# Optimization experiments

Measured on AMD Instinct MI355X. Metric: run time of the kernel, lower is better.

Reference implementation:

```python
import jax, jax.numpy as jnp
import numpy as np

NUM_CLASSES = 21
RMI_RADIUS = 3
POOL = 3            # rmi_pool_size == rmi_pool_stride
HALF_D = RMI_RADIUS * RMI_RADIUS
WEIGHT_LAMBDA = 0.5
CLIP_MIN = 1e-6
POS_ALPHA = 5e-4


def _max_pool(x):
    # F.max_pool2d(kernel=3, stride=3, padding=1) on NCHW
    return jax.lax.reduce_window(
        x, -jnp.inf, jax.lax.max,
        window_dimensions=(1, 1, POOL, POOL),
        window_strides=(1, 1, POOL, POOL),
        padding=[(0, 0), (0, 0), (1, 1), (1, 1)])


def _map_get_pairs(labels, probs, radius):
    # -> two tensors [N, C, radius*radius, new_h, new_w]
    h, w = labels.shape[2], labels.shape[3]
    nh, nw = h - (radius - 1), w - (radius - 1)
    la = jnp.stack([labels[:, :, y:y + nh, x:x + nw]
                    for y in range(radius) for x in range(radius)], axis=2)
    pr = jnp.stack([probs[:, :, y:y + nh, x:x + nw]
                    for y in range(radius) for x in range(radius)], axis=2)
    return la, pr


def _rmi_lower_bound(labels_4D, probs_4D):
    labels_4D = _max_pool(labels_4D)
    probs_4D = _max_pool(probs_4D)
    la, pr = _map_get_pairs(labels_4D, probs_4D, RMI_RADIUS)
    N, C = la.shape[0], la.shape[1]
    la = jax.lax.stop_gradient(la.reshape(N, C, HALF_D, -1))  # [N,C,D,M]
    pr = pr.reshape(N, C, HALF_D, -1)
    la = la - jnp.mean(la, axis=3, keepdims=True)
    pr = pr - jnp.mean(pr, axis=3, keepdims=True)
    eye = jnp.eye(HALF_D, dtype=pr.dtype) * POS_ALPHA  # broadcast over N,C
    la_cov = jnp.einsum('ncdm,ncem->ncde', la, la)
    pr_cov = jnp.einsum('ncdm,ncem->ncde', pr, pr)
    pr_cov_inv = jnp.linalg.inv(pr_cov + eye)
    la_pr_cov = jnp.einsum('ncdm,ncem->ncde', la, pr)
    appro_var = la_cov - jnp.einsum('ncde,ncef,ncgf->ncdg',
                                    la_pr_cov, pr_cov_inv, la_pr_cov)
    chol = jnp.linalg.cholesky(appro_var + eye)
    diag = jnp.diagonal(chol, axis1=-2, axis2=-1)
    rmi_now = 0.5 * 2.0 * jnp.sum(jnp.log(diag + 1e-8), axis=-1)  # [N,C]
    rmi_per_class = jnp.mean(rmi_now.reshape(-1, NUM_CLASSES), axis=0) / float(HALF_D)
    return jnp.sum(rmi_per_class)  # _IS_SUM = 1


def setup_inputs() -> dict:
    key = jax.random.key(0)
    k1, k2 = jax.random.split(key)
    logits_4D = jax.random.normal(k1, (4, NUM_CLASSES, 512, 512), dtype=jnp.float32)
    labels_4D = jax.random.randint(k2, (4, 512, 512), 0, NUM_CLASSES).astype(jnp.int64)
    return {'logits_4D': logits_4D, 'labels_4D': labels_4D}


def reference(logits_4D, labels_4D):
    # forward_sigmoid
    mask = (labels_4D < NUM_CLASSES)                       # [N,H,W] bool
    maskf = mask.astype(logits_4D.dtype)
    onehot = jax.nn.one_hot(labels_4D * mask, NUM_CLASSES,
                            dtype=logits_4D.dtype) * maskf[..., None]  # [N,H,W,C]
    onehot = jax.lax.stop_gradient(onehot)
    logits_flat = jnp.transpose(logits_4D, (0, 2, 3, 1)).reshape(-1, NUM_CLASSES)
    y_flat = onehot.reshape(-1, NUM_CLASSES)
    w_flat = maskf.reshape(-1, 1)
    valid_pixels = jnp.sum(maskf)
    # stable BCE-with-logits, sum reduction, per-pixel weight
    bce = -(y_flat * jax.nn.log_sigmoid(logits_flat)
            + (1.0 - y_flat) * jax.nn.log_sigmoid(-logits_flat))
    bce_loss = jnp.sum(bce * w_flat) / (valid_pixels + 1.0)
    probs_4D = jax.nn.sigmoid(logits_4D) * maskf[:, None, :, :] + CLIP_MIN
    labels_nchw = jnp.transpose(onehot, (0, 3, 1, 2))
    rmi_loss = _rmi_lower_bound(labels_nchw, probs_4D)
    # lambda_way == 1
    return WEIGHT_LAMBDA * bce_loss + rmi_loss * (1.0 - WEIGHT_LAMBDA)
```

## Files before the change

kernel.cpp:

```cpp
#include <hip/hip_runtime.h>
#include <math.h>
#include <stdint.h>

#define NUM_CL 21
#define NB 4
#define H 512
#define W 512
#define PH 171
#define PW 171
#define PWPAD 176
#define NHH 169
#define NWW 169
#define M_TOT (NHH*NWW)
#define NCP (NB*NUM_CL)
#define ACC_PAD 192
#define POS_ALPHA 5e-4
#define NBLKA (NB*NUM_CL*PH)
#define NROWBLK (NB*PH)
#define SEGR 43

typedef unsigned long long u64;
typedef unsigned int u32;

__device__ __forceinline__ int upIdx(int lo, int hi) {
    return lo*9 - (lo*(lo-1))/2 + (hi - lo);
}
__device__ __forceinline__ int tri(int d, int e) { return d*(d+1)/2 + e; }

__device__ __forceinline__ float wred64(float v) {
    #pragma unroll
    for (int o = 32; o > 0; o >>= 1) v += __shfl_down(v, o, 64);
    return v;
}

__global__ __launch_bounds__(128) void kernelA(
    const float* __restrict__ logits, const int* __restrict__ labels,
    float* __restrict__ pooledP, unsigned char* __restrict__ pooledL8,
    float* __restrict__ bce_part, u32* __restrict__ cnt_part)
{
    int blk = blockIdx.x;
    int c  = blk % NUM_CL;
    int t2 = blk / NUM_CL;
    int ph = t2 % PH;
    int n  = t2 / PH;
    int tid = threadIdx.x;
    int col0 = tid << 2;

    __shared__ float         svP[W];
    __shared__ unsigned char svL[W];
    __shared__ float         rbce[2];
    __shared__ u32           rcnt[2];

    const float* lgp = logits + (size_t)(n*NUM_CL + c) * (H*W);
    const int*   lbp = labels + (size_t)n * (H*W);

    float vP[4] = {-INFINITY, -INFINITY, -INFINITY, -INFINITY};
    int   vL[4] = {0,0,0,0};
    float bce = 0.f;
    u32 cnt = 0;

    int rbase = 3*ph - 1;
    #pragma unroll
    for (int rr = 0; rr < 3; ++rr) {
        int r = rbase + rr;
        if (r < 0 || r >= H) continue;
        float4 x4 = *(const float4*)(lgp + (size_t)r*W + col0);
        int4   l4 = *(const int4*)  (lbp + (size_t)r*W + col0);
        float xs[4] = {x4.x, x4.y, x4.z, x4.w};
        int   ls[4] = {l4.x, l4.y, l4.z, l4.w};
        #pragma unroll
        for (int k = 0; k < 4; ++k) {
            int lab = ls[k];
            float x = xs[k];
            float m = (lab < NUM_CL) ? 1.f : 0.f;
            float y = (lab == c) ? 1.f : 0.f;
            float te = __expf(-fabsf(x));
            float u  = 1.f + te;
            float sp = __logf(u);
            float rc = __builtin_amdgcn_rcpf(u);
            bce += m * (fmaxf(x, 0.f) - x*y + sp);
            float sig = (x >= 0.f) ? rc : te*rc;
            vP[k] = fmaxf(vP[k], sig*m + 1e-6f);
            vL[k] |= (lab == c);
            cnt += (u32)(lab < NUM_CL);
        }
    }

    ((float4*)svP)[tid] = make_float4(vP[0], vP[1], vP[2], vP[3]);
    uchar4 u4;
    u4.x = (unsigned char)vL[0]; u4.y = (unsigned char)vL[1];
    u4.z = (unsigned char)vL[2]; u4.w = (unsigned char)vL[3];
    ((uchar4*)svL)[tid] = u4;

    #pragma unroll
    for (int o = 32; o > 0; o >>= 1) {
        bce += __shfl_down(bce, o, 64);
        cnt += __shfl_down(cnt, o, 64);
    }
    int lane = tid & 63, wv = tid >> 6;
    if (lane == 0) { rbce[wv] = bce; rcnt[wv] = cnt; }
    __syncthreads();

    size_t rowr = (size_t)(n*NUM_CL + c) * PH + ph;
    #pragma unroll
    for (int pass = 0; pass < 2; ++pass) {
        int pw = tid + pass*128;
        if (pw < PW) {
            int c0 = 3*pw - 1; if (c0 < 0) c0 = 0;
            int c1 = 3*pw + 2; if (c1 > W) c1 = W;
            float pm = -INFINITY;
            int lm = 0;
            for (int qq = c0; qq < c1; ++qq) {
                pm = fmaxf(pm, svP[qq]);
                lm |= svL[qq];
            }
            pooledP [rowr * PWPAD + pw] = pm;
            pooledL8[rowr * PWPAD + pw] = (unsigned char)lm;
        }
    }

    if (tid == 0) {
        bce_part[blk] = rbce[0] + rbce[1];
        if (c == 0) cnt_part[t2] = rcnt[0] + rcnt[1];
    }
}

template<int CNT>
__device__ __forceinline__ void blockReduceStore(
    float (&v)[CNT], float* __restrict__ stage, int off, bool active,
    int lane, int wave)
{
    __shared__ float red[4][CNT];
    #pragma unroll
    for (int k = 0; k < CNT; ++k) {
        float r = wred64(active ? v[k] : 0.f);
        if (lane == 0) red[wave][k] = r;
    }
    __syncthreads();
    for (int k = (int)threadIdx.x; k < CNT; k += 256) {
        stage[off + k] = red[0][k] + red[1][k] + red[2][k] + red[3][k];
    }
    __syncthreads();
}

__global__ __launch_bounds__(256, 1) void kernelB(
    const float* __restrict__ pooledP, const unsigned char* __restrict__ pooledL8,
    float* __restrict__ stage)
{
    int nc    = blockIdx.x;
    int chunk = blockIdx.y;
    int grp   = blockIdx.z;
    int lane  = threadIdx.x & 63;
    int seg   = threadIdx.x >> 6;
    int j     = chunk*64 + lane;
    bool active = (j < NWW);
    int jc = active ? j : (NWW - 1);
    int i0 = seg * SEGR;
    int i1 = (seg == 3) ? NWW : (i0 + SEGR);

    const float* P = pooledP + (size_t)nc * PH * PWPAD + jc;
    const unsigned char* L = pooledL8 + (size_t)nc * PH * PWPAD + jc;
    float* st = stage + (size_t)(nc*3 + chunk) * ACC_PAD;

    float pA[3], pB[3], lA[3], lB[3];
    #pragma unroll
    for (int t = 0; t < 3; ++t) {
        pA[t] = P[(size_t)i0 * PWPAD + t];
        lA[t] = (float)L[(size_t)i0 * PWPAD + t];
        pB[t] = P[(size_t)(i0+1) * PWPAD + t];
        lB[t] = (float)L[(size_t)(i0+1) * PWPAD + t];
    }

    if (grp == 0) {
        float sl[9], sp[9], cll[45], cpp[45];
        #pragma unroll
        for (int d = 0; d < 9; ++d) { sl[d] = 0.f; sp[d] = 0.f; }
        #pragma unroll
        for (int k = 0; k < 45; ++k) { cll[k] = 0.f; cpp[k] = 0.f; }

        for (int i = i0; i < i1; ++i) {
            const float* rp = P + (size_t)(i+2) * PWPAD;
            const unsigned char* rl = L + (size_t)(i+2) * PWPAD;
            float pC[3] = {rp[0], rp[1], rp[2]};
            float lC[3] = {(float)rl[0], (float)rl[1], (float)rl[2]};
            float pv[9] = {pA[0],pA[1],pA[2], pB[0],pB[1],pB[2], pC[0],pC[1],pC[2]};
            float lv[9] = {lA[0],lA[1],lA[2], lB[0],lB[1],lB[2], lC[0],lC[1],lC[2]};
            #pragma unroll
            for (int d = 0; d < 9; ++d) { sp[d] += pv[d]; sl[d] += lv[d]; }
            int k = 0;
            #pragma unroll
            for (int d = 0; d < 9; ++d)
                #pragma unroll
                for (int e = d; e < 9; ++e) {
                    cpp[k] += pv[d]*pv[e];
                    cll[k] += lv[d]*lv[e];
                    ++k;
                }
            #pragma unroll
            for (int t = 0; t < 3; ++t) {
                pA[t] = pB[t]; pB[t] = pC[t];
                lA[t] = lB[t]; lB[t] = lC[t];
            }
        }
        blockReduceStore<9> (sl,  st, 0,  active, lane, seg);
        blockReduceStore<9> (sp,  st, 9,  active, lane, seg);
        blockReduceStore<45>(cll, st, 18, active, lane, seg);
        blockReduceStore<45>(cpp, st, 63, active, lane, seg);
    } else {
        float clp[81];
        #pragma unroll
        for (int k = 0; k < 81; ++k) clp[k] = 0.f;

        for (int i = i0; i < i1; ++i) {
            const float* rp = P + (size_t)(i+2) * PWPAD;
            const unsigned char* rl = L + (size_t)(i+2) * PWPAD;
            float pC[3] = {rp[0], rp[1], rp[2]};
            float lC[3] = {(float)rl[0], (float)rl[1], (float)rl[2]};
            float pv[9] = {pA[0],pA[1],pA[2], pB[0],pB[1],pB[2], pC[0],pC[1],pC[2]};
            float lv[9] = {lA[0],lA[1],lA[2], lB[0],lB[1],lB[2], lC[0],lC[1],lC[2]};
            #pragma unroll
            for (int d = 0; d < 9; ++d)
                #pragma unroll
                for (int e = 0; e < 9; ++e)
                    clp[d*9+e] += lv[d]*pv[e];
            #pragma unroll
            for (int t = 0; t < 3; ++t) {
                pA[t] = pB[t]; pB[t] = pC[t];
                lA[t] = lB[t]; lB[t] = lC[t];
            }
        }
        blockReduceStore<81>(clp, st, 108, active, lane, seg);
    }
}

__device__ __forceinline__ double rdacc(const float* __restrict__ st, int t, int k) {
    const float* b = st + (size_t)t * 3 * ACC_PAD + k;
    return (double)b[0] + (double)b[ACC_PAD] + (double)b[2*ACC_PAD];
}

__global__ __launch_bounds__(256) void kernelC(
    const float* __restrict__ stage,
    const float* __restrict__ bce_part,
    const u32* __restrict__ cnt_part,
    float* __restrict__ out)
{
    int t = threadIdx.x;

    __shared__ double sb[256];
    __shared__ u32 sc[256];
    double bs = 0.0;
    for (int i = t; i < NBLKA; i += 256) bs += (double)bce_part[i];
    u32 cs = 0;
    for (int i = t; i < NROWBLK; i += 256) cs += cnt_part[i];
    sb[t] = bs; sc[t] = cs;
    __syncthreads();
    #pragma unroll
    for (int s = 128; s > 0; s >>= 1) {
        if (t < s) { sb[t] += sb[t + s]; sc[t] += sc[t + s]; }
        __syncthreads();
    }

    float contrib = 0.f;
    if (t < NCP) {
        const double Minv = 1.0 / (double)M_TOT;
        double Sl[9], Sp[9];
        #pragma unroll
        for (int d = 0; d < 9; ++d) { Sl[d] = rdacc(stage, t, d); Sp[d] = rdacc(stage, t, 9+d); }

        float A[45];
        float G[45];
        float B[81];
        #pragma unroll
        for (int d = 0; d < 9; ++d) {
            #pragma unroll
            for (int e = 0; e <= d; ++e) {
                int ku = upIdx(e, d);
                double vp = rdacc(stage, t, 63+ku) - Sp[d]*Sp[e]*Minv;
                double vl = rdacc(stage, t, 18+ku) - Sl[d]*Sl[e]*Minv;
                if (d == e) vp += POS_ALPHA;
                A[tri(d,e)] = (float)vp;
                G[tri(d,e)] = (float)vl;
            }
        }
        #pragma unroll
        for (int d = 0; d < 9; ++d) {
            #pragma unroll
            for (int e = 0; e < 9; ++e)
                B[d*9+e] = (float)(rdacc(stage, t, 108 + d*9 + e) - Sl[d]*Sp[e]*Minv);
        }

        #pragma unroll
        for (int d = 0; d < 9; ++d) {
            float s = A[tri(d,d)];
            #pragma unroll
            for (int f = 0; f < d; ++f) { float v = A[tri(d,f)]; s -= v*v; }
            float ldd = sqrtf(s);
            A[tri(d,d)] = ldd;
            float inv = 1.f / ldd;
            #pragma unroll
            for (int e = d+1; e < 9; ++e) {
                float s2 = A[tri(e,d)];
                #pragma unroll
                for (int f = 0; f < d; ++f) s2 -= A[tri(e,f)] * A[tri(d,f)];
                A[tri(e,d)] = s2 * inv;
            }
        }

        #pragma unroll
        for (int d = 0; d < 9; ++d) {
            #pragma unroll
            for (int e = 0; e < 9; ++e) {
                float s = B[d*9+e];
                #pragma unroll
                for (int f = 0; f < e; ++f) s -= A[tri(e,f)] * B[d*9+f];
                B[d*9+e] = s / A[tri(e,e)];
            }
        }

        #pragma unroll
        for (int d = 0; d < 9; ++d) {
            #pragma unroll
            for (int g = 0; g <= d; ++g) {
                float qv = 0.f;
                #pragma unroll
                for (int e = 0; e < 9; ++e) qv += B[d*9+e] * B[g*9+e];
                float v = G[tri(d,g)] - qv;
                if (d == g) v += (float)POS_ALPHA;
                G[tri(d,g)] = v;
            }
        }

        float sumlog = 0.f;
        #pragma unroll
        for (int d = 0; d < 9; ++d) {
            float s = G[tri(d,d)];
            #pragma unroll
            for (int f = 0; f < d; ++f) { float v = G[tri(d,f)]; s -= v*v; }
            float ldd = sqrtf(s);
            G[tri(d,d)] = ldd;
            sumlog += logf(ldd + 1e-8f);
            float inv = 1.f / ldd;
            #pragma unroll
            for (int e = d+1; e < 9; ++e) {
                float s2 = G[tri(e,d)];
                #pragma unroll
                for (int f = 0; f < d; ++f) s2 -= G[tri(e,f)] * G[tri(d,f)];
                G[tri(e,d)] = s2 * inv;
            }
        }
        contrib = sumlog * (1.0f / 36.0f);
    }

    __shared__ float sred[256];
    sred[t] = contrib;
    __syncthreads();
    #pragma unroll
    for (int s = 128; s > 0; s >>= 1) {
        if (t < s) sred[t] += sred[t + s];
        __syncthreads();
    }
    if (t == 0) {
        double bce_loss = sb[0] / ((double)sc[0] + 1.0);
        out[0] = (float)(0.5 * bce_loss + 0.5 * (double)sred[0]);
    }
}

extern "C" void kernel_launch(void* const* d_in, const int* in_sizes, int n_in,
                              void* d_out, int out_size, void* d_ws, size_t ws_size,
                              hipStream_t stream)
{
    (void)in_sizes; (void)n_in; (void)out_size; (void)ws_size;
    const float* logits = (const float*)d_in[0];
    const int*   labels = (const int*)d_in[1];
    float* out = (float*)d_out;

    uint8_t* w = (uint8_t*)d_ws;
    size_t off = 0;
    float* stage = (float*)(w + off);          off += (size_t)NCP * 3 * ACC_PAD * 4;
    float* bce_part = (float*)(w + off);       off += (size_t)NBLKA * 4;
    u32* cnt_part = (u32*)(w + off);           off += (size_t)NROWBLK * 4;
    off = (off + 15) & ~(size_t)15;
    float* pooledP = (float*)(w + off);        off += (size_t)NCP * PH * PWPAD * 4;
    unsigned char* pooledL8 = (unsigned char*)(w + off); off += (size_t)NCP * PH * PWPAD;

    kernelA<<<NBLKA, 128, 0, stream>>>(logits, labels, pooledP, pooledL8, bce_part, cnt_part);
    kernelB<<<dim3(NCP, 3, 2), 256, 0, stream>>>(pooledP, pooledL8, stage);
    kernelC<<<1, 256, 0, stream>>>(stage, bce_part, cnt_part, out);
}
```

Measured before the change: 209.8 us.

## Fuse three kernels into one persistent kernel with software grid barriers

```diff
diff --git a/kernel.cpp b/kernel.cpp
--- a/kernel.cpp
+++ b/kernel.cpp
@@ -16,8 +16,9 @@
 #define ACC_PAD 192
 #define POS_ALPHA 5e-4
 #define NBLKA (NB*NUM_CL*PH)
-#define NROWBLK (NB*PH)
 #define SEGR 43
+#define GRID 256
+#define AITERS ((NBLKA + GRID*2 - 1) / (GRID*2))
 
 typedef unsigned long long u64;
 typedef unsigned int u32;
@@ -33,335 +34,362 @@
     return v;
 }
 
-__global__ __launch_bounds__(128) void kernelA(
-    const float* __restrict__ logits, const int* __restrict__ labels,
-    float* __restrict__ pooledP, unsigned char* __restrict__ pooledL8,
-    float* __restrict__ bce_part, u32* __restrict__ cnt_part)
-{
-    int blk = blockIdx.x;
-    int c  = blk % NUM_CL;
-    int t2 = blk / NUM_CL;
-    int ph = t2 % PH;
-    int n  = t2 / PH;
-    int tid = threadIdx.x;
-    int col0 = tid << 2;
-
-    __shared__ float         svP[W];
-    __shared__ unsigned char svL[W];
-    __shared__ float         rbce[2];
-    __shared__ u32           rcnt[2];
-
-    const float* lgp = logits + (size_t)(n*NUM_CL + c) * (H*W);
-    const int*   lbp = labels + (size_t)n * (H*W);
-
-    float vP[4] = {-INFINITY, -INFINITY, -INFINITY, -INFINITY};
-    int   vL[4] = {0,0,0,0};
-    float bce = 0.f;
-    u32 cnt = 0;
-
-    int rbase = 3*ph - 1;
-    #pragma unroll
-    for (int rr = 0; rr < 3; ++rr) {
-        int r = rbase + rr;
-        if (r < 0 || r >= H) continue;
-        float4 x4 = *(const float4*)(lgp + (size_t)r*W + col0);
-        int4   l4 = *(const int4*)  (lbp + (size_t)r*W + col0);
-        float xs[4] = {x4.x, x4.y, x4.z, x4.w};
-        int   ls[4] = {l4.x, l4.y, l4.z, l4.w};
-        #pragma unroll
-        for (int k = 0; k < 4; ++k) {
-            int lab = ls[k];
-            float x = xs[k];
-            float m = (lab < NUM_CL) ? 1.f : 0.f;
-            float y = (lab == c) ? 1.f : 0.f;
-            float te = __expf(-fabsf(x));
-            float u  = 1.f + te;
-            float sp = __logf(u);
-            float rc = __builtin_amdgcn_rcpf(u);
-            bce += m * (fmaxf(x, 0.f) - x*y + sp);
-            float sig = (x >= 0.f) ? rc : te*rc;
-            vP[k] = fmaxf(vP[k], sig*m + 1e-6f);
-            vL[k] |= (lab == c);
-            cnt += (u32)(lab < NUM_CL);
-        }
-    }
-
-    ((float4*)svP)[tid] = make_float4(vP[0], vP[1], vP[2], vP[3]);
-    uchar4 u4;
-    u4.x = (unsigned char)vL[0]; u4.y = (unsigned char)vL[1];
-    u4.z = (unsigned char)vL[2]; u4.w = (unsigned char)vL[3];
-    ((uchar4*)svL)[tid] = u4;
-
-    #pragma unroll
-    for (int o = 32; o > 0; o >>= 1) {
-        bce += __shfl_down(bce, o, 64);
-        cnt += __shfl_down(cnt, o, 64);
-    }
-    int lane = tid & 63, wv = tid >> 6;
-    if (lane == 0) { rbce[wv] = bce; rcnt[wv] = cnt; }
-    __syncthreads();
-
-    size_t rowr = (size_t)(n*NUM_CL + c) * PH + ph;
-    #pragma unroll
-    for (int pass = 0; pass < 2; ++pass) {
-        int pw = tid + pass*128;
-        if (pw < PW) {
-            int c0 = 3*pw - 1; if (c0 < 0) c0 = 0;
-            int c1 = 3*pw + 2; if (c1 > W) c1 = W;
-            float pm = -INFINITY;
-            int lm = 0;
-            for (int qq = c0; qq < c1; ++qq) {
-                pm = fmaxf(pm, svP[qq]);
-                lm |= svL[qq];
-            }
-            pooledP [rowr * PWPAD + pw] = pm;
-            pooledL8[rowr * PWPAD + pw] = (unsigned char)lm;
-        }
-    }
-
-    if (tid == 0) {
-        bce_part[blk] = rbce[0] + rbce[1];
-        if (c == 0) cnt_part[t2] = rcnt[0] + rcnt[1];
-    }
-}
-
-template<int CNT>
-__device__ __forceinline__ void blockReduceStore(
-    float (&v)[CNT], float* __restrict__ stage, int off, bool active,
-    int lane, int wave)
-{
-    __shared__ float red[4][CNT];
-    #pragma unroll
-    for (int k = 0; k < CNT; ++k) {
-        float r = wred64(active ? v[k] : 0.f);
-        if (lane == 0) red[wave][k] = r;
-    }
-    __syncthreads();
-    for (int k = (int)threadIdx.x; k < CNT; k += 256) {
-        stage[off + k] = red[0][k] + red[1][k] + red[2][k] + red[3][k];
-    }
-    __syncthreads();
-}
-
-__global__ __launch_bounds__(256, 1) void kernelB(
-    const float* __restrict__ pooledP, const unsigned char* __restrict__ pooledL8,
-    float* __restrict__ stage)
-{
-    int nc    = blockIdx.x;
-    int chunk = blockIdx.y;
-    int grp   = blockIdx.z;
-    int lane  = threadIdx.x & 63;
-    int seg   = threadIdx.x >> 6;
-    int j     = chunk*64 + lane;
-    bool active = (j < NWW);
-    int jc = active ? j : (NWW - 1);
-    int i0 = seg * SEGR;
-    int i1 = (seg == 3) ? NWW : (i0 + SEGR);
-
-    const float* P = pooledP + (size_t)nc * PH * PWPAD + jc;
-    const unsigned char* L = pooledL8 + (size_t)nc * PH * PWPAD + jc;
-    float* st = stage + (size_t)(nc*3 + chunk) * ACC_PAD;
-
-    float pA[3], pB[3], lA[3], lB[3];
-    #pragma unroll
-    for (int t = 0; t < 3; ++t) {
-        pA[t] = P[(size_t)i0 * PWPAD + t];
-        lA[t] = (float)L[(size_t)i0 * PWPAD + t];
-        pB[t] = P[(size_t)(i0+1) * PWPAD + t];
-        lB[t] = (float)L[(size_t)(i0+1) * PWPAD + t];
-    }
-
-    if (grp == 0) {
-        float sl[9], sp[9], cll[45], cpp[45];
-        #pragma unroll
-        for (int d = 0; d < 9; ++d) { sl[d] = 0.f; sp[d] = 0.f; }
-        #pragma unroll
-        for (int k = 0; k < 45; ++k) { cll[k] = 0.f; cpp[k] = 0.f; }
-
-        for (int i = i0; i < i1; ++i) {
-            const float* rp = P + (size_t)(i+2) * PWPAD;
-            const unsigned char* rl = L + (size_t)(i+2) * PWPAD;
-            float pC[3] = {rp[0], rp[1], rp[2]};
-            float lC[3] = {(float)rl[0], (float)rl[1], (float)rl[2]};
-            float pv[9] = {pA[0],pA[1],pA[2], pB[0],pB[1],pB[2], pC[0],pC[1],pC[2]};
-            float lv[9] = {lA[0],lA[1],lA[2], lB[0],lB[1],lB[2], lC[0],lC[1],lC[2]};
-            #pragma unroll
-            for (int d = 0; d < 9; ++d) { sp[d] += pv[d]; sl[d] += lv[d]; }
-            int k = 0;
-            #pragma unroll
-            for (int d = 0; d < 9; ++d)
-                #pragma unroll
-                for (int e = d; e < 9; ++e) {
-                    cpp[k] += pv[d]*pv[e];
-                    cll[k] += lv[d]*lv[e];
-                    ++k;
-                }
-            #pragma unroll
-            for (int t = 0; t < 3; ++t) {
-                pA[t] = pB[t]; pB[t] = pC[t];
-                lA[t] = lB[t]; lB[t] = lC[t];
-            }
-        }
-        blockReduceStore<9> (sl,  st, 0,  active, lane, seg);
-        blockReduceStore<9> (sp,  st, 9,  active, lane, seg);
-        blockReduceStore<45>(cll, st, 18, active, lane, seg);
-        blockReduceStore<45>(cpp, st, 63, active, lane, seg);
-    } else {
-        float clp[81];
-        #pragma unroll
-        for (int k = 0; k < 81; ++k) clp[k] = 0.f;
-
-        for (int i = i0; i < i1; ++i) {
-            const float* rp = P + (size_t)(i+2) * PWPAD;
-            const unsigned char* rl = L + (size_t)(i+2) * PWPAD;
-            float pC[3] = {rp[0], rp[1], rp[2]};
-            float lC[3] = {(float)rl[0], (float)rl[1], (float)rl[2]};
-            float pv[9] = {pA[0],pA[1],pA[2], pB[0],pB[1],pB[2], pC[0],pC[1],pC[2]};
-            float lv[9] = {lA[0],lA[1],lA[2], lB[0],lB[1],lB[2], lC[0],lC[1],lC[2]};
-            #pragma unroll
-            for (int d = 0; d < 9; ++d)
-                #pragma unroll
-                for (int e = 0; e < 9; ++e)
-                    clp[d*9+e] += lv[d]*pv[e];
-            #pragma unroll
-            for (int t = 0; t < 3; ++t) {
-                pA[t] = pB[t]; pB[t] = pC[t];
-                lA[t] = lB[t]; lB[t] = lC[t];
-            }
-        }
-        blockReduceStore<81>(clp, st, 108, active, lane, seg);
-    }
-}
-
 __device__ __forceinline__ double rdacc(const float* __restrict__ st, int t, int k) {
     const float* b = st + (size_t)t * 3 * ACC_PAD + k;
     return (double)b[0] + (double)b[ACC_PAD] + (double)b[2*ACC_PAD];
 }
 
-__global__ __launch_bounds__(256) void kernelC(
-    const float* __restrict__ stage,
-    const float* __restrict__ bce_part,
-    const u32* __restrict__ cnt_part,
+__device__ __forceinline__ void gridBarrier(u32* cnt, u32* rel) {
+    __syncthreads();
+    if (threadIdx.x == 0) {
+        __threadfence();
+        u32 old = __hip_atomic_fetch_add(cnt, 1u, __ATOMIC_ACQ_REL, __HIP_MEMORY_SCOPE_AGENT);
+        if (old == GRID - 1) {
+            __hip_atomic_store(rel, 1u, __ATOMIC_RELEASE, __HIP_MEMORY_SCOPE_AGENT);
+        } else {
+            while (__hip_atomic_load(rel, __ATOMIC_ACQUIRE, __HIP_MEMORY_SCOPE_AGENT) == 0u) {
+                __builtin_amdgcn_s_sleep(8);
+            }
+        }
+        __threadfence();
+    }
+    __syncthreads();
+}
+
+__global__ __launch_bounds__(256, 2) void mega(
+    const float* __restrict__ logits, const int* __restrict__ labels,
+    float* __restrict__ pooledP, unsigned char* __restrict__ pooledL8,
+    float* __restrict__ stage, float* __restrict__ bce_part,
+    u32* __restrict__ cnt_part, u32* __restrict__ bar,
     float* __restrict__ out)
 {
-    int t = threadIdx.x;
-
-    __shared__ double sb[256];
-    __shared__ u32 sc[256];
-    double bs = 0.0;
-    for (int i = t; i < NBLKA; i += 256) bs += (double)bce_part[i];
-    u32 cs = 0;
-    for (int i = t; i < NROWBLK; i += 256) cs += cnt_part[i];
-    sb[t] = bs; sc[t] = cs;
+    int tid  = threadIdx.x;
+    int half = tid >> 7;
+    int th   = tid & 127;
+
+    __shared__ float         svP[2][W];
+    __shared__ unsigned char svL[2][W];
+    __shared__ float         rb[256];
+    __shared__ u32           rc[256];
+    __shared__ float         red[4][108];
+
+    float bce = 0.f;
+    u32 cnt = 0;
+
+    for (int it = 0; it < AITERS; ++it) {
+        int task = (it*GRID + (int)blockIdx.x)*2 + half;
+        bool act = task < NBLKA;
+        int c = 0;
+        size_t rowr = 0;
+        float4 x4[3]; int4 l4[3];
+        int rbase = 0;
+        if (act) {
+            c = task % NUM_CL;
+            int t2 = task / NUM_CL;
+            int ph = t2 % PH;
+            int n  = t2 / PH;
+            rowr = (size_t)(n*NUM_CL + c) * PH + ph;
+            const float* lgp = logits + (size_t)(n*NUM_CL + c) * (H*W);
+            const int*   lbp = labels + (size_t)n * (H*W);
+            rbase = 3*ph - 1;
+            int col0 = th << 2;
+            #pragma unroll
+            for (int rr = 0; rr < 3; ++rr) {
+                int r = rbase + rr;
+                if (r >= 0) {
+                    x4[rr] = *(const float4*)(lgp + (size_t)r*W + col0);
+                    l4[rr] = *(const int4*)  (lbp + (size_t)r*W + col0);
+                }
+            }
+        }
+
+        float vP[4] = {-INFINITY, -INFINITY, -INFINITY, -INFINITY};
+        int   vL[4] = {0,0,0,0};
+        if (act) {
+            #pragma unroll
+            for (int rr = 0; rr < 3; ++rr) {
+                int r = rbase + rr;
+                if (r < 0) continue;
+                float xs[4] = {x4[rr].x, x4[rr].y, x4[rr].z, x4[rr].w};
+                int   ls[4] = {l4[rr].x, l4[rr].y, l4[rr].z, l4[rr].w};
+                #pragma unroll
+                for (int k = 0; k < 4; ++k) {
+                    int lab = ls[k];
+                    float x = xs[k];
+                    float m = (lab < NUM_CL) ? 1.f : 0.f;
+                    float y = (lab == c) ? 1.f : 0.f;
+                    float te = __expf(-fabsf(x));
+                    float u  = 1.f + te;
+                    float sp = __logf(u);
+                    float rcv = __builtin_amdgcn_rcpf(u);
+                    bce += m * (fmaxf(x, 0.f) - x*y + sp);
+                    float sig = (x >= 0.f) ? rcv : te*rcv;
+                    vP[k] = fmaxf(vP[k], sig*m + 1e-6f);
+                    vL[k] |= (lab == c);
+                    if (c == 0) cnt += (u32)(lab < NUM_CL);
+                }
+            }
+            ((float4*)svP[half])[th] = make_float4(vP[0], vP[1], vP[2], vP[3]);
+            uchar4 u4;
+            u4.x = (unsigned char)vL[0]; u4.y = (unsigned char)vL[1];
+            u4.z = (unsigned char)vL[2]; u4.w = (unsigned char)vL[3];
+            ((uchar4*)svL[half])[th] = u4;
+        }
+        __syncthreads();
+        if (act) {
+            #pragma unroll
+            for (int pass = 0; pass < 2; ++pass) {
+                int pw = th + pass*128;
+                if (pw < PW) {
+                    int c0 = 3*pw - 1; if (c0 < 0) c0 = 0;
+                    int c1 = 3*pw + 2; if (c1 > W) c1 = W;
+                    float pm = -INFINITY;
+                    int lm = 0;
+                    for (int qq = c0; qq < c1; ++qq) {
+                        pm = fmaxf(pm, svP[half][qq]);
+                        lm |= svL[half][qq];
+                    }
+                    pooledP [rowr * PWPAD + pw] = pm;
+                    pooledL8[rowr * PWPAD + pw] = (unsigned char)lm;
+                }
+            }
+        }
+        __syncthreads();
+    }
+
+    rb[tid] = bce; rc[tid] = cnt;
     __syncthreads();
     #pragma unroll
     for (int s = 128; s > 0; s >>= 1) {
-        if (t < s) { sb[t] += sb[t + s]; sc[t] += sc[t + s]; }
+        if (tid < s) { rb[tid] += rb[tid + s]; rc[tid] += rc[tid + s]; }
         __syncthreads();
     }
-
-    float contrib = 0.f;
-    if (t < NCP) {
-        const double Minv = 1.0 / (double)M_TOT;
-        double Sl[9], Sp[9];
+    if (tid == 0) { bce_part[blockIdx.x] = rb[0]; cnt_part[blockIdx.x] = rc[0]; }
+
+    gridBarrier(&bar[0], &bar[1]);
+
+    for (int btask = (int)blockIdx.x; btask < NCP*6; btask += GRID) {
+        int nc    = btask / 6;
+        int rem   = btask - nc*6;
+        int chunk = rem % 3;
+        int grp   = rem / 3;
+        int lane  = tid & 63;
+        int seg   = tid >> 6;
+        int j     = chunk*64 + lane;
+        bool active = (j < NWW);
+        int jc = active ? j : (NWW - 1);
+        int i0 = seg * SEGR;
+        int i1 = (seg == 3) ? NWW : (i0 + SEGR);
+
+        const float* P = pooledP + (size_t)nc * PH * PWPAD + jc;
+        const unsigned char* L = pooledL8 + (size_t)nc * PH * PWPAD + jc;
+        float* st = stage + (size_t)(nc*3 + chunk) * ACC_PAD;
+
+        float pA[3], pB[3], lA[3], lB[3];
         #pragma unroll
-        for (int d = 0; d < 9; ++d) { Sl[d] = rdacc(stage, t, d); Sp[d] = rdacc(stage, t, 9+d); }
-
-        float A[45];
-        float G[45];
-        float B[81];
+        for (int t = 0; t < 3; ++t) {
+            pA[t] = P[(size_t)i0 * PWPAD + t];
+            lA[t] = (float)L[(size_t)i0 * PWPAD + t];
+            pB[t] = P[(size_t)(i0+1) * PWPAD + t];
+            lB[t] = (float)L[(size_t)(i0+1) * PWPAD + t];
+        }
+
+        if (grp == 0) {
+            float sl[9], sp[9], cll[45], cpp[45];
+            #pragma unroll
+            for (int d = 0; d < 9; ++d) { sl[d] = 0.f; sp[d] = 0.f; }
+            #pragma unroll
+            for (int k = 0; k < 45; ++k) { cll[k] = 0.f; cpp[k] = 0.f; }
+
+            for (int i = i0; i < i1; ++i) {
+                const float* rp = P + (size_t)(i+2) * PWPAD;
+                const unsigned char* rl = L + (size_t)(i+2) * PWPAD;
+                float pC[3] = {rp[0], rp[1], rp[2]};
+                float lC[3] = {(float)rl[0], (float)rl[1], (float)rl[2]};
+                float pv[9] = {pA[0],pA[1],pA[2], pB[0],pB[1],pB[2], pC[0],pC[1],pC[2]};
+                float lv[9] = {lA[0],lA[1],lA[2], lB[0],lB[1],lB[2], lC[0],lC[1],lC[2]};
+                #pragma unroll
+                for (int d = 0; d < 9; ++d) { sp[d] += pv[d]; sl[d] += lv[d]; }
+                int k = 0;
+                #pragma unroll
+                for (int d = 0; d < 9; ++d)
+                    #pragma unroll
+                    for (int e = d; e < 9; ++e) {
+                        cpp[k] += pv[d]*pv[e];
+                        cll[k] += lv[d]*lv[e];
+                        ++k;
+                    }
+                #pragma unroll
+                for (int t = 0; t < 3; ++t) {
+                    pA[t] = pB[t]; pB[t] = pC[t];
+                    lA[t] = lB[t]; lB[t] = lC[t];
+                }
+            }
+            #pragma unroll
+            for (int k = 0; k < 9; ++k) { float r = wred64(active ? sl[k] : 0.f); if (lane == 0) red[seg][k] = r; }
+            #pragma unroll
+            for (int k = 0; k < 9; ++k) { float r = wred64(active ? sp[k] : 0.f); if (lane == 0) red[seg][9+k] = r; }
+            #pragma unroll
+            for (int k = 0; k < 45; ++k) { float r = wred64(active ? cll[k] : 0.f); if (lane == 0) red[seg][18+k] = r; }
+            __syncthreads();
+            for (int k = tid; k < 63; k += 256)
+                st[k] = red[0][k] + red[1][k] + red[2][k] + red[3][k];
+            __syncthreads();
+            #pragma unroll
+            for (int k = 0; k < 45; ++k) { float r = wred64(active ? cpp[k] : 0.f); if (lane == 0) red[seg][k] = r; }
+            __syncthreads();
+            for (int k = tid; k < 45; k += 256)
+                st[63 + k] = red[0][k] + red[1][k] + red[2][k] + red[3][k];
+            __syncthreads();
+        } else {
+            float clp[81];
+            #pragma unroll
+            for (int k = 0; k < 81; ++k) clp[k] = 0.f;
+
+            for (int i = i0; i < i1; ++i) {
+                const float* rp = P + (size_t)(i+2) * PWPAD;
+                const unsigned char* rl = L + (size_t)(i+2) * PWPAD;
+                float pC[3] = {rp[0], rp[1], rp[2]};
+                float lC[3] = {(float)rl[0], (float)rl[1], (float)rl[2]};
+                float pv[9] = {pA[0],pA[1],pA[2], pB[0],pB[1],pB[2], pC[0],pC[1],pC[2]};
+                float lv[9] = {lA[0],lA[1],lA[2], lB[0],lB[1],lB[2], lC[0],lC[1],lC[2]};
+                #pragma unroll
+                for (int d = 0; d < 9; ++d)
+                    #pragma unroll
+                    for (int e = 0; e < 9; ++e)
+                        clp[d*9+e] += lv[d]*pv[e];
+                #pragma unroll
+                for (int t = 0; t < 3; ++t) {
+                    pA[t] = pB[t]; pB[t] = pC[t];
+                    lA[t] = lB[t]; lB[t] = lC[t];
+                }
+            }
+            #pragma unroll
+            for (int k = 0; k < 81; ++k) { float r = wred64(active ? clp[k] : 0.f); if (lane == 0) red[seg][k] = r; }
+            __syncthreads();
+            for (int k = tid; k < 81; k += 256)
+                st[108 + k] = red[0][k] + red[1][k] + red[2][k] + red[3][k];
+            __syncthreads();
+        }
+    }
+
+    gridBarrier(&bar[2], &bar[3]);
+
+    if (blockIdx.x == 0) {
+        int t = tid;
+        __shared__ double sb[256];
+        __shared__ u32 sc2[256];
+        double bs = 0.0; u32 cs = 0;
+        for (int i = t; i < GRID; i += 256) { bs += (double)bce_part[i]; cs += cnt_part[i]; }
+        sb[t] = bs; sc2[t] = cs;
+        __syncthreads();
         #pragma unroll
-        for (int d = 0; d < 9; ++d) {
-            #pragma unroll
-            for (int e = 0; e <= d; ++e) {
-                int ku = upIdx(e, d);
-                double vp = rdacc(stage, t, 63+ku) - Sp[d]*Sp[e]*Minv;
-                double vl = rdacc(stage, t, 18+ku) - Sl[d]*Sl[e]*Minv;
-                if (d == e) vp += POS_ALPHA;
-                A[tri(d,e)] = (float)vp;
-                G[tri(d,e)] = (float)vl;
-            }
-        }
+        for (int s = 128; s > 0; s >>= 1) {
+            if (t < s) { sb[t] += sb[t + s]; sc2[t] += sc2[t + s]; }
+            __syncthreads();
+        }
+
+        float contrib = 0.f;
+        if (t < NCP) {
+            const double Minv = 1.0 / (double)M_TOT;
+            double Sl[9], Sp[9];
+            #pragma unroll
+            for (int d = 0; d < 9; ++d) { Sl[d] = rdacc(stage, t, d); Sp[d] = rdacc(stage, t, 9+d); }
+
+            float A[45], G[45], B[81];
+            #pragma unroll
+            for (int d = 0; d < 9; ++d) {
+                #pragma unroll
+                for (int e = 0; e <= d; ++e) {
+                    int ku = upIdx(e, d);
+                    double vp = rdacc(stage, t, 63+ku) - Sp[d]*Sp[e]*Minv;
+                    double vl = rdacc(stage, t, 18+ku) - Sl[d]*Sl[e]*Minv;
+                    if (d == e) vp += POS_ALPHA;
+                    A[tri(d,e)] = (float)vp;
+                    G[tri(d,e)] = (float)vl;
+                }
+            }
+            #pragma unroll
+            for (int d = 0; d < 9; ++d) {
+                #pragma unroll
+                for (int e = 0; e < 9; ++e)
+                    B[d*9+e] = (float)(rdacc(stage, t, 108 + d*9 + e) - Sl[d]*Sp[e]*Minv);
+            }
+
+            #pragma unroll
+            for (int d = 0; d < 9; ++d) {
+                float s = A[tri(d,d)];
+                #pragma unroll
+                for (int f = 0; f < d; ++f) { float v = A[tri(d,f)]; s -= v*v; }
+                float ldd = sqrtf(s);
+                A[tri(d,d)] = ldd;
+                float inv = 1.f / ldd;
+                #pragma unroll
+                for (int e = d+1; e < 9; ++e) {
+                    float s2 = A[tri(e,d)];
+                    #pragma unroll
+                    for (int f = 0; f < d; ++f) s2 -= A[tri(e,f)] * A[tri(d,f)];
+                    A[tri(e,d)] = s2 * inv;
+                }
+            }
+
+            #pragma unroll
+            for (int d = 0; d < 9; ++d) {
+                #pragma unroll
+                for (int e = 0; e < 9; ++e) {
+                    float s = B[d*9+e];
+                    #pragma unroll
+                    for (int f = 0; f < e; ++f) s -= A[tri(e,f)] * B[d*9+f];
+                    B[d*9+e] = s / A[tri(e,e)];
+                }
+            }
+
+            #pragma unroll
+            for (int d = 0; d < 9; ++d) {
+                #pragma unroll
+                for (int g = 0; g <= d; ++g) {
+                    float qv = 0.f;
+                    #pragma unroll
+                    for (int e = 0; e < 9; ++e) qv += B[d*9+e] * B[g*9+e];
+                    float v = G[tri(d,g)] - qv;
+                    if (d == g) v += (float)POS_ALPHA;
+                    G[tri(d,g)] = v;
+                }
+            }
+
+            float sumlog = 0.f;
+            #pragma unroll
+            for (int d = 0; d < 9; ++d) {
+                float s = G[tri(d,d)];
+                #pragma unroll
+                for (int f = 0; f < d; ++f) { float v = G[tri(d,f)]; s -= v*v; }
+                float ldd = sqrtf(s);
+                G[tri(d,d)] = ldd;
+                sumlog += logf(ldd + 1e-8f);
+                float inv = 1.f / ldd;
+                #pragma unroll
+                for (int e = d+1; e < 9; ++e) {
+                    float s2 = G[tri(e,d)];
+                    #pragma unroll
+                    for (int f = 0; f < d; ++f) s2 -= G[tri(e,f)] * G[tri(d,f)];
+                    G[tri(e,d)] = s2 * inv;
+                }
+            }
+            contrib = sumlog * (1.0f / 36.0f);
+        }
+
+        __shared__ float sred[256];
+        sred[t] = contrib;
+        __syncthreads();
         #pragma unroll
-        for (int d = 0; d < 9; ++d) {
-            #pragma unroll
-            for (int e = 0; e < 9; ++e)
-                B[d*9+e] = (float)(rdacc(stage, t, 108 + d*9 + e) - Sl[d]*Sp[e]*Minv);
-        }
-
-        #pragma unroll
-        for (int d = 0; d < 9; ++d) {
-            float s = A[tri(d,d)];
-            #pragma unroll
-            for (int f = 0; f < d; ++f) { float v = A[tri(d,f)]; s -= v*v; }
-            float ldd = sqrtf(s);
-            A[tri(d,d)] = ldd;
-            float inv = 1.f / ldd;
-            #pragma unroll
-            for (int e = d+1; e < 9; ++e) {
-                float s2 = A[tri(e,d)];
-                #pragma unroll
-                for (int f = 0; f < d; ++f) s2 -= A[tri(e,f)] * A[tri(d,f)];
-                A[tri(e,d)] = s2 * inv;
-            }
-        }
-
-        #pragma unroll
-        for (int d = 0; d < 9; ++d) {
-            #pragma unroll
-            for (int e = 0; e < 9; ++e) {
-                float s = B[d*9+e];
-                #pragma unroll
-                for (int f = 0; f < e; ++f) s -= A[tri(e,f)] * B[d*9+f];
-                B[d*9+e] = s / A[tri(e,e)];
-            }
-        }
-
-        #pragma unroll
-        for (int d = 0; d < 9; ++d) {
-            #pragma unroll
-            for (int g = 0; g <= d; ++g) {
-                float qv = 0.f;
-                #pragma unroll
-                for (int e = 0; e < 9; ++e) qv += B[d*9+e] * B[g*9+e];
-                float v = G[tri(d,g)] - qv;
-                if (d == g) v += (float)POS_ALPHA;
-                G[tri(d,g)] = v;
-            }
-        }
-
-        float sumlog = 0.f;
-        #pragma unroll
-        for (int d = 0; d < 9; ++d) {
-            float s = G[tri(d,d)];
-            #pragma unroll
-            for (int f = 0; f < d; ++f) { float v = G[tri(d,f)]; s -= v*v; }
-            float ldd = sqrtf(s);
-            G[tri(d,d)] = ldd;
-            sumlog += logf(ldd + 1e-8f);
-            float inv = 1.f / ldd;
-            #pragma unroll
-            for (int e = d+1; e < 9; ++e) {
-                float s2 = G[tri(e,d)];
-                #pragma unroll
-                for (int f = 0; f < d; ++f) s2 -= G[tri(e,f)] * G[tri(d,f)];
-                G[tri(e,d)] = s2 * inv;
-            }
-        }
-        contrib = sumlog * (1.0f / 36.0f);
-    }
-
-    __shared__ float sred[256];
-    sred[t] = contrib;
-    __syncthreads();
-    #pragma unroll
-    for (int s = 128; s > 0; s >>= 1) {
-        if (t < s) sred[t] += sred[t + s];
-        __syncthreads();
-    }
-    if (t == 0) {
-        double bce_loss = sb[0] / ((double)sc[0] + 1.0);
-        out[0] = (float)(0.5 * bce_loss + 0.5 * (double)sred[0]);
+        for (int s = 128; s > 0; s >>= 1) {
+            if (t < s) sred[t] += sred[t + s];
+            __syncthreads();
+        }
+        if (t == 0) {
+            double bce_loss = sb[0] / ((double)sc2[0] + 1.0);
+            out[0] = (float)(0.5 * bce_loss + 0.5 * (double)sred[0]);
+        }
     }
 }
 
@@ -376,14 +404,15 @@
 
     uint8_t* w = (uint8_t*)d_ws;
     size_t off = 0;
+    u32* bar = (u32*)(w + off);                off += 64;
     float* stage = (float*)(w + off);          off += (size_t)NCP * 3 * ACC_PAD * 4;
-    float* bce_part = (float*)(w + off);       off += (size_t)NBLKA * 4;
-    u32* cnt_part = (u32*)(w + off);           off += (size_t)NROWBLK * 4;
+    float* bce_part = (float*)(w + off);       off += (size_t)GRID * 4;
+    u32* cnt_part = (u32*)(w + off);           off += (size_t)GRID * 4;
     off = (off + 15) & ~(size_t)15;
     float* pooledP = (float*)(w + off);        off += (size_t)NCP * PH * PWPAD * 4;
     unsigned char* pooledL8 = (unsigned char*)(w + off); off += (size_t)NCP * PH * PWPAD;
 
-    kernelA<<<NBLKA, 128, 0, stream>>>(logits, labels, pooledP, pooledL8, bce_part, cnt_part);
-    kernelB<<<dim3(NCP, 3, 2), 256, 0, stream>>>(pooledP, pooledL8, stage);
-    kernelC<<<1, 256, 0, stream>>>(stage, bce_part, cnt_part, out);
-}
+    hipMemsetAsync(bar, 0, 64, stream);
+    mega<<<GRID, 256, 0, stream>>>(logits, labels, pooledP, pooledL8,
+                                   stage, bce_part, cnt_part, bar, out);
+}
```

Result: slower. 371.0 us (+76.8%).
